# Optimization experiments

Hardware: AMD Instinct MI355X
Metric: run time of the kernel (lower is better)

The kernel has to match this reference:

```python
import jax, jax.numpy as jnp
import numpy as np

N_NODES = 100000
N_EDGES = 1200000
D = 64          # node_feat_size
G_FEAT = 128    # graph_feat_size
N_GRAPHS = 256
N_TASKS = 1


def setup_inputs() -> dict:
    key = jax.random.key(0)
    ks = jax.random.split(key, 12)
    node_feats = jax.random.normal(ks[0], (N_NODES, D), dtype=jnp.float32)
    edge_feats = jax.random.normal(ks[1], (N_EDGES, 8), dtype=jnp.float32)
    src = jax.random.randint(ks[2], (N_EDGES,), 0, N_NODES, dtype=jnp.int64 if jax.config.read('jax_enable_x64') else jnp.int32)
    dst = jax.random.randint(ks[3], (N_EDGES,), 0, N_NODES, dtype=src.dtype)
    graph_ids = jnp.sort(jax.random.randint(ks[4], (N_NODES,), 0, N_GRAPHS, dtype=src.dtype))
    s = 1.0 / np.sqrt(D)
    W_gcn = jax.random.uniform(ks[5], (D, D), minval=-s, maxval=s, dtype=jnp.float32)
    b_gcn = jnp.zeros((D,), jnp.float32)
    W_res = jax.random.uniform(ks[6], (D, D), minval=-s, maxval=s, dtype=jnp.float32)
    b_res = jnp.zeros((D,), jnp.float32)
    W_in = jax.random.uniform(ks[7], (D, D), minval=-s, maxval=s, dtype=jnp.float32)
    b_in = jnp.zeros((D,), jnp.float32)
    W_out = jax.random.uniform(ks[8], (D, G_FEAT), minval=-s, maxval=s, dtype=jnp.float32)
    b_out = jnp.zeros((G_FEAT,), jnp.float32)
    sp = 1.0 / np.sqrt(G_FEAT)
    W_pred = jax.random.uniform(ks[9], (G_FEAT, N_TASKS), minval=-sp, maxval=sp, dtype=jnp.float32)
    b_pred = jnp.zeros((N_TASKS,), jnp.float32)
    return dict(node_feats=node_feats, edge_feats=edge_feats, src=src, dst=dst,
                graph_ids=graph_ids, W_gcn=W_gcn, b_gcn=b_gcn, W_res=W_res, b_res=b_res,
                W_in=W_in, b_in=b_in, W_out=W_out, b_out=b_out, W_pred=W_pred, b_pred=b_pred)


def reference(node_feats, edge_feats, src, dst, graph_ids,
              W_gcn, b_gcn, W_res, b_res, W_in, b_in, W_out, b_out, W_pred, b_pred):
    # --- GCNLayer (GraphConv norm='none', activation=relu, residual=True) ---
    # message passing: copy src features, sum at dst (no normalization)
    agg = jax.ops.segment_sum(node_feats[src], dst, num_segments=N_NODES)  # [N, D]
    h = jax.nn.relu(agg @ W_gcn + b_gcn)                                   # graph_conv output
    h = h + jax.nn.relu(node_feats @ W_res + b_res)                        # residual branch
    # --- MLPNodeReadout (mode='sum') ---
    h = jax.nn.relu(h @ W_in + b_in)      # [N, D]
    h = h @ W_out + b_out                 # [N, G_FEAT]
    g_feats = jax.ops.segment_sum(h, graph_ids, num_segments=N_GRAPHS)  # [G, G_FEAT]
    # --- predict ---
    out = (g_feats @ W_pred + b_pred).reshape(-1)  # [G * n_tasks]
    return out
```

## Files before the change

### kernel.cpp

```cpp
#include <hip/hip_runtime.h>

typedef __attribute__((ext_vector_type(8))) __bf16 bf16x8;
typedef __attribute__((ext_vector_type(4))) float f32x4;

union Frag { unsigned short u[8]; bf16x8 b; };

__device__ __forceinline__ unsigned short rne_bf16(float x) {
    unsigned int u = __float_as_uint(x);
    return (unsigned short)((u + 0x7fffu + ((u >> 16) & 1u)) >> 16);
}
__device__ __forceinline__ float bf16_to_f(unsigned short h) {
    return __uint_as_float(((unsigned int)h) << 16);
}

#define MFMA16 __builtin_amdgcn_mfma_f32_16x16x32_bf16
#define SBSH 9
#define SBN 512
#define SBCAP 7168
#define BINCHUNK 4096
#define NWFRAG (3 * 2 * 2 * 4 * 64 * 8)

__global__ __launch_bounds__(256) void bin_kernel(
    const int* __restrict__ src, const int* __restrict__ dst,
    int* __restrict__ gcursor, int* __restrict__ binned,
    int nE, int nbS) {
    __shared__ int lhist[256], lbase[256], lofs[256];
    __shared__ int wsum[4];
    __shared__ int sortedV[BINCHUNK];
    __shared__ int sortedA[BINCHUNK];
    const int t = threadIdx.x;
    const int e0 = blockIdx.x * BINCHUNK;
    const int e1 = min(e0 + BINCHUNK, nE);
    const int cnt = e1 - e0;
    lhist[t] = 0;
    __syncthreads();
    int myr[16];
    #pragma unroll
    for (int u = 0; u < 16; ++u) {
        int e = e0 + t + u * 256;
        if (e < e1) myr[u] = atomicAdd(&lhist[dst[e] >> SBSH], 1);
    }
    __syncthreads();
    const int lane = t & 63, w = t >> 6;
    int x = lhist[t];
    #pragma unroll
    for (int s = 1; s < 64; s <<= 1) {
        int v = __shfl_up(x, s, 64);
        if (lane >= s) x += v;
    }
    if (lane == 63) wsum[w] = x;
    __syncthreads();
    if (t < 4) {
        int y = wsum[t];
        #pragma unroll
        for (int s = 1; s < 4; s <<= 1) {
            int v = __shfl_up(y, s, 64);
            if (t >= s) y += v;
        }
        wsum[t] = y;
    }
    __syncthreads();
    lofs[t] = x + (w ? wsum[w - 1] : 0);
    if (t < nbS) {
        int c = lhist[t];
        lbase[t] = c ? atomicAdd(&gcursor[t], c) : 0;
    }
    __syncthreads();
    #pragma unroll
    for (int u = 0; u < 16; ++u) {
        int e = e0 + t + u * 256;
        if (e < e1) {
            int d = dst[e];
            int sb = d >> SBSH;
            int r = myr[u];
            int p = (lofs[sb] - lhist[sb]) + r;
            sortedV[p] = (src[e] << SBSH) | (d & (SBN - 1));
            int gp = lbase[sb] + r;
            sortedA[p] = (gp < SBCAP) ? (sb * SBCAP + gp) : -1;
        }
    }
    __syncthreads();
    for (int i = t; i < cnt; i += 256) {
        int ga = sortedA[i];
        if (ga >= 0) binned[ga] = sortedV[i];
    }
}

__global__ __launch_bounds__(1024) void segB_kernel(
    int* __restrict__ binned, const int* __restrict__ gcursor,
    int2* __restrict__ nodeTab,
    const float* __restrict__ nf,
    const float* __restrict__ Wg, const float* __restrict__ Wr,
    const float* __restrict__ Wi, const float* __restrict__ Wo,
    const float* __restrict__ bo, const float* __restrict__ Wp,
    const float* __restrict__ bp,
    unsigned short* __restrict__ nfb, unsigned short* __restrict__ wfrag,
    float* __restrict__ wfold, float* __restrict__ c0, float* __restrict__ out,
    int nbS, int out_size, int nNodes) {
    __shared__ int eL[SBCAP];
    __shared__ int deg[SBN], sc[SBN];
    __shared__ int wsum[8];
    const int b = blockIdx.x, t = threadIdx.x;
    if (b < nbS) {
        const int cnt = min(gcursor[b], SBCAP);
        const int bb = b * SBCAP;
        if (t < SBN) deg[t] = 0;
        __syncthreads();
        int myr[7];
        #pragma unroll
        for (int u = 0; u < 7; ++u) {
            int i = t + u * 1024;
            if (i < cnt) {
                int p = binned[bb + i];
                eL[i] = p;
                myr[u] = atomicAdd(&deg[p & (SBN - 1)], 1);
            }
        }
        __syncthreads();
        const int lane = t & 63, w = t >> 6;
        if (t < SBN) {
            int d = deg[t];
            int x = d;
            #pragma unroll
            for (int s = 1; s < 64; s <<= 1) {
                int v = __shfl_up(x, s, 64);
                if (lane >= s) x += v;
            }
            if (lane == 63) wsum[w] = x;
            __syncthreads();
            if (t < 8) {
                int y = wsum[t];
                #pragma unroll
                for (int s = 1; s < 8; s <<= 1) {
                    int v = __shfl_up(y, s, 64);
                    if (t >= s) y += v;
                }
                wsum[t] = y;
            }
            __syncthreads();
            int incl = x + (w ? wsum[w - 1] : 0);
            int excl = incl - d;
            sc[t] = excl;
            int node = b * SBN + t;
            if (node < nNodes) nodeTab[node] = make_int2(bb + excl, d);
        } else {
            __syncthreads();
            __syncthreads();
        }
        __syncthreads();
        #pragma unroll
        for (int u = 0; u < 7; ++u) {
            int i = t + u * 1024;
            if (i < cnt) {
                int p = eL[i];
                int pos = sc[p & (SBN - 1)] + myr[u];
                binned[bb + pos] = p >> SBSH;
            }
        }
        return;
    }
    const int tp = ((int)blockIdx.x - nbS) * 1024 + t;
    const int nth = ((int)gridDim.x - nbS) * 1024;
    const float4* nf4 = (const float4*)nf;
    ushort4* nfb4 = (ushort4*)nfb;
    const int nQ = nNodes * 16;
    for (int i = tp; i < nQ; i += nth) {
        float4 v = nf4[i];
        ushort4 o;
        o.x = rne_bf16(v.x); o.y = rne_bf16(v.y);
        o.z = rne_bf16(v.z); o.w = rne_bf16(v.w);
        nfb4[i] = o;
    }
    const float* Ws[3] = {Wg, Wr, Wi};
    for (int idx = tp; idx < NWFRAG; idx += nth) {
        int j = idx & 7, lane = (idx >> 3) & 63, nt = (idx >> 9) & 3;
        int kt = (idx >> 11) & 1, part = (idx >> 12) & 1, mat = idx >> 13;
        int k = kt * 32 + ((lane >> 4) << 3) + j;
        int n = nt * 16 + (lane & 15);
        float ww = Ws[mat][k * 64 + n];
        unsigned short hi = rne_bf16(ww);
        wfrag[idx] = (part == 0) ? hi : rne_bf16(ww - bf16_to_f(hi));
    }
    if (tp < 64) {
        float s = 0.f;
        for (int j = 0; j < 128; ++j) s += Wo[tp * 128 + j] * Wp[j];
        wfold[tp] = s;
    }
    if (tp == 0) {
        float s = 0.f;
        for (int j = 0; j < 128; ++j) s += bo[j] * Wp[j];
        c0[0] = s;
    }
    if (tp < out_size) out[tp] = bp[0];
}

__global__ __launch_bounds__(256) void gather_kernel(
    const unsigned short* __restrict__ nfb, const int2* __restrict__ nodeTab,
    const int* __restrict__ srcs, unsigned short* __restrict__ aggb, int nNodes) {
    int wid = blockIdx.x * 4 + (threadIdx.x >> 6);
    if (wid >= nNodes) return;
    int lane = threadIdx.x & 63;
    int half = lane >> 5;
    int cp = lane & 31;
    int2 sd = nodeTab[wid];
    int base = sd.x, d = sd.y;
    const ushort2* nfb2 = (const ushort2*)nfb;
    float ax = 0.f, ay = 0.f;
    if (d > 0 && d <= 64) {
        int myidx = srcs[base + min(lane, d - 1)];
        int dh = (d - half + 1) >> 1;
        for (int jb = 0; jb < dh; jb += 8) {
            int sA[8];
            #pragma unroll
            for (int u = 0; u < 8; ++u) {
                int e = 2 * (jb + u) + half;
                sA[u] = __shfl(myidx, (e < d) ? e : (d - 1), 64);
            }
            ushort2 v[8];
            #pragma unroll
            for (int u = 0; u < 8; ++u)
                v[u] = nfb2[(long)sA[u] * 32 + cp];
            #pragma unroll
            for (int u = 0; u < 8; ++u)
                if (jb + u < dh) { ax += bf16_to_f(v[u].x); ay += bf16_to_f(v[u].y); }
        }
    } else if (d > 64) {
        int k = half;
        for (; k + 8 <= d; k += 8) {
            int s0 = srcs[base + k],     s1 = srcs[base + k + 2];
            int s2 = srcs[base + k + 4], s3 = srcs[base + k + 6];
            ushort2 v0 = nfb2[(long)s0 * 32 + cp];
            ushort2 v1 = nfb2[(long)s1 * 32 + cp];
            ushort2 v2 = nfb2[(long)s2 * 32 + cp];
            ushort2 v3 = nfb2[(long)s3 * 32 + cp];
            ax += (bf16_to_f(v0.x) + bf16_to_f(v1.x)) + (bf16_to_f(v2.x) + bf16_to_f(v3.x));
            ay += (bf16_to_f(v0.y) + bf16_to_f(v1.y)) + (bf16_to_f(v2.y) + bf16_to_f(v3.y));
        }
        for (; k < d; k += 2) {
            int s = srcs[base + k];
            ushort2 v = nfb2[(long)s * 32 + cp];
            ax += bf16_to_f(v.x); ay += bf16_to_f(v.y);
        }
    }
    ax += __shfl_xor(ax, 32, 64);
    ay += __shfl_xor(ay, 32, 64);
    if (half == 0) {
        ushort2 o; o.x = rne_bf16(ax); o.y = rne_bf16(ay);
        ((ushort2*)aggb)[(long)wid * 32 + cp] = o;
    }
}

__global__ __launch_bounds__(256) void mlp_kernel(
    const unsigned short* __restrict__ aggb, const unsigned short* __restrict__ nfb,
    const int* __restrict__ gids, const unsigned short* __restrict__ wfrag,
    const float* __restrict__ bg, const float* __restrict__ br,
    const float* __restrict__ bi, const float* __restrict__ wfold,
    const float* __restrict__ c0p, float* __restrict__ out, int nTiles) {
    __shared__ float hs_all[4][32 * 68];
    const int wave = threadIdx.x >> 6, lane = threadIdx.x & 63;
    const int wid = blockIdx.x * 4 + wave;
    if (wid >= nTiles) return;
    float* hs = hs_all[wave];
    const int base = wid * 32;
    const int mrow = lane & 15, quad = lane >> 4;

    Frag aA[2][2], aN[2][2];
    #pragma unroll
    for (int rt = 0; rt < 2; ++rt) {
        const unsigned short* rowA = aggb + (long)(base + rt * 16 + mrow) * 64;
        const unsigned short* rowN = nfb  + (long)(base + rt * 16 + mrow) * 64;
        #pragma unroll
        for (int kt = 0; kt < 2; ++kt) {
            aA[rt][kt].b = *(const bf16x8*)(rowA + kt * 32 + quad * 8);
            aN[rt][kt].b = *(const bf16x8*)(rowN + kt * 32 + quad * 8);
        }
    }
    const unsigned short* wl0 = wfrag + lane * 8;
    auto WF = [&](int mat, int part, int kt, int nt) -> bf16x8 {
        return *(const bf16x8*)(wl0 + (size_t)((((mat * 2 + part) * 2 + kt) * 4 + nt) * 64) * 8);
    };
    f32x4 accA[2][4], accR[2][4];
    #pragma unroll
    for (int rt = 0; rt < 2; ++rt)
        #pragma unroll
        for (int nt = 0; nt < 4; ++nt) {
            accA[rt][nt] = (f32x4){0.f, 0.f, 0.f, 0.f};
            accR[rt][nt] = (f32x4){0.f, 0.f, 0.f, 0.f};
        }
    #pragma unroll
    for (int nt = 0; nt < 4; ++nt)
        #pragma unroll
        for (int kt = 0; kt < 2; ++kt) {
            bf16x8 gh = WF(0, 0, kt, nt), gl = WF(0, 1, kt, nt);
            bf16x8 rh = WF(1, 0, kt, nt), rl = WF(1, 1, kt, nt);
            #pragma unroll
            for (int rt = 0; rt < 2; ++rt) {
                accA[rt][nt] = MFMA16(aA[rt][kt].b, gh, accA[rt][nt], 0, 0, 0);
                accA[rt][nt] = MFMA16(aA[rt][kt].b, gl, accA[rt][nt], 0, 0, 0);
                accR[rt][nt] = MFMA16(aN[rt][kt].b, rh, accR[rt][nt], 0, 0, 0);
                accR[rt][nt] = MFMA16(aN[rt][kt].b, rl, accR[rt][nt], 0, 0, 0);
            }
        }
    #pragma unroll
    for (int nt = 0; nt < 4; ++nt) {
        float bgv = bg[nt * 16 + mrow], brv = br[nt * 16 + mrow];
        #pragma unroll
        for (int rt = 0; rt < 2; ++rt)
            #pragma unroll
            for (int r = 0; r < 4; ++r) {
                float h = fmaxf(accA[rt][nt][r] + bgv, 0.f)
                        + fmaxf(accR[rt][nt][r] + brv, 0.f);
                hs[(rt * 16 + quad * 4 + r) * 68 + nt * 16 + mrow] = h;
            }
    }
    __builtin_amdgcn_wave_barrier();
    Frag aH[2][2];
    #pragma unroll
    for (int rt = 0; rt < 2; ++rt)
        #pragma unroll
        for (int kt = 0; kt < 2; ++kt) {
            const float* hp = hs + (rt * 16 + mrow) * 68 + kt * 32 + quad * 8;
            float4 v0 = *(const float4*)hp;
            float4 v1 = *(const float4*)(hp + 4);
            aH[rt][kt].u[0] = rne_bf16(v0.x); aH[rt][kt].u[1] = rne_bf16(v0.y);
            aH[rt][kt].u[2] = rne_bf16(v0.z); aH[rt][kt].u[3] = rne_bf16(v0.w);
            aH[rt][kt].u[4] = rne_bf16(v1.x); aH[rt][kt].u[5] = rne_bf16(v1.y);
            aH[rt][kt].u[6] = rne_bf16(v1.z); aH[rt][kt].u[7] = rne_bf16(v1.w);
        }
    f32x4 accH[2][4];
    #pragma unroll
    for (int rt = 0; rt < 2; ++rt)
        #pragma unroll
        for (int nt = 0; nt < 4; ++nt)
            accH[rt][nt] = (f32x4){0.f, 0.f, 0.f, 0.f};
    #pragma unroll
    for (int nt = 0; nt < 4; ++nt)
        #pragma unroll
        for (int kt = 0; kt < 2; ++kt) {
            bf16x8 ih = WF(2, 0, kt, nt), il = WF(2, 1, kt, nt);
            #pragma unroll
            for (int rt = 0; rt < 2; ++rt) {
                accH[rt][nt] = MFMA16(aH[rt][kt].b, ih, accH[rt][nt], 0, 0, 0);
                accH[rt][nt] = MFMA16(aH[rt][kt].b, il, accH[rt][nt], 0, 0, 0);
            }
        }
    float p[2][4];
    #pragma unroll
    for (int rt = 0; rt < 2; ++rt)
        #pragma unroll
        for (int r = 0; r < 4; ++r) p[rt][r] = 0.f;
    #pragma unroll
    for (int nt = 0; nt < 4; ++nt) {
        float biv = bi[nt * 16 + mrow], wfv = wfold[nt * 16 + mrow];
        #pragma unroll
        for (int rt = 0; rt < 2; ++rt)
            #pragma unroll
            for (int r = 0; r < 4; ++r)
                p[rt][r] += fmaxf(accH[rt][nt][r] + biv, 0.f) * wfv;
    }
    #pragma unroll
    for (int m = 1; m <= 8; m <<= 1)
        #pragma unroll
        for (int rt = 0; rt < 2; ++rt)
            #pragma unroll
            for (int r = 0; r < 4; ++r)
                p[rt][r] += __shfl_xor(p[rt][r], m, 64);
    const float c0 = c0p[0];
    #pragma unroll
    for (int rt = 0; rt < 2; ++rt)
        #pragma unroll
        for (int r = 0; r < 4; ++r) p[rt][r] += c0;
    int gself = gids[base + (lane & 31)];
    int g0 = __shfl(gself, 0, 64);
    if (__all(gself == g0)) {
        float pv = 0.f;
        if (mrow == 0) {
            #pragma unroll
            for (int rt = 0; rt < 2; ++rt)
                #pragma unroll
                for (int r = 0; r < 4; ++r) pv += p[rt][r];
        }
        pv += __shfl_xor(pv, 16, 64);
        pv += __shfl_xor(pv, 32, 64);
        if (lane == 0) atomicAdd(out + g0, pv);
    } else if (mrow == 0) {
        #pragma unroll
        for (int rt = 0; rt < 2; ++rt)
            #pragma unroll
            for (int r = 0; r < 4; ++r)
                atomicAdd(out + gids[base + rt * 16 + quad * 4 + r], p[rt][r]);
    }
}

extern "C" void kernel_launch(void* const* d_in, const int* in_sizes, int n_in,
                              void* d_out, int out_size, void* d_ws, size_t ws_size,
                              hipStream_t stream) {
    const float* node_feats = (const float*)d_in[0];
    const int* src  = (const int*)d_in[2];
    const int* dst  = (const int*)d_in[3];
    const int* gids = (const int*)d_in[4];
    const float* Wg = (const float*)d_in[5];
    const float* bg = (const float*)d_in[6];
    const float* Wr = (const float*)d_in[7];
    const float* br = (const float*)d_in[8];
    const float* Wi = (const float*)d_in[9];
    const float* bi = (const float*)d_in[10];
    const float* Wo = (const float*)d_in[11];
    const float* bo = (const float*)d_in[12];
    const float* Wp = (const float*)d_in[13];
    const float* bp = (const float*)d_in[14];
    float* out = (float*)d_out;

    const int nNodes = in_sizes[0] / 64;
    const int nE = in_sizes[2];
    const int nbS = (nNodes + SBN - 1) / SBN;
    const int nBin = (nE + BINCHUNK - 1) / BINCHUNK;
    const int nTiles = (nNodes + 31) / 32;

    int* gcursor = (int*)d_ws;
    int* binned  = gcursor + 256;
    int2* nodeTab = (int2*)(binned + (size_t)nbS * SBCAP);
    unsigned short* nfb  = (unsigned short*)(nodeTab + nNodes);
    unsigned short* aggb = nfb + (size_t)nNodes * 64;
    unsigned short* wfrag = aggb + (size_t)nNodes * 64;
    float* wfold = (float*)(wfrag + NWFRAG);
    float* c0 = wfold + 64;

    hipMemsetAsync(gcursor, 0, 256 * sizeof(int), stream);

    bin_kernel<<<nBin, 256, 0, stream>>>(src, dst, gcursor, binned, nE, nbS);

    segB_kernel<<<nbS + 256, 1024, 0, stream>>>(binned, gcursor, nodeTab,
        node_feats, Wg, Wr, Wi, Wo, bo, Wp, bp,
        nfb, wfrag, wfold, c0, out, nbS, out_size, nNodes);

    gather_kernel<<<(nNodes + 3) / 4, 256, 0, stream>>>(nfb, nodeTab, binned, aggb, nNodes);

    mlp_kernel<<<(nTiles + 3) / 4, 256, 0, stream>>>(aggb, nfb, gids, wfrag,
        bg, br, bi, wfold, c0, out, nTiles);
}
```

Before: 210.2 us.

## Fuse binning, segment sort, gather and MLP into one cooperative persistent kernel

Replaces the memset plus four separate kernel launches with a single cooperative kernel that runs each phase in grid-stride loops, separated by grid-wide syncs. Shared memory is reused across phases through a union. The gather phase now handles two nodes per wave, and the segment phase runs with 256 threads instead of 1024. This removes launch overhead and inter-kernel gaps, but adds grid.sync costs, caps occupancy at the cooperative grid size, and changes the per-phase parallelism.

```diff
diff --git a/kernel.cpp b/kernel.cpp
--- a/kernel.cpp
+++ b/kernel.cpp
@@ -1,4 +1,7 @@
 #include <hip/hip_runtime.h>
+#include <hip/hip_cooperative_groups.h>
+
+namespace cg = cooperative_groups;
 
 typedef __attribute__((ext_vector_type(8))) __bf16 bf16x8;
 typedef __attribute__((ext_vector_type(4))) float f32x4;
@@ -20,375 +23,394 @@
 #define BINCHUNK 4096
 #define NWFRAG (3 * 2 * 2 * 4 * 64 * 8)
 
-__global__ __launch_bounds__(256) void bin_kernel(
-    const int* __restrict__ src, const int* __restrict__ dst,
-    int* __restrict__ gcursor, int* __restrict__ binned,
-    int nE, int nbS) {
-    __shared__ int lhist[256], lbase[256], lofs[256];
-    __shared__ int wsum[4];
-    __shared__ int sortedV[BINCHUNK];
-    __shared__ int sortedA[BINCHUNK];
+struct KArgs {
+    const float* nf; const int* src; const int* dst; const int* gids;
+    const float* Wg; const float* bg; const float* Wr; const float* br;
+    const float* Wi; const float* bi; const float* Wo; const float* bo;
+    const float* Wp; const float* bp;
+    float* out;
+    int* gcursor; int* binned; int2* nodeTab;
+    unsigned short* nfb; unsigned short* aggb; unsigned short* wfrag;
+    float* wfold; float* c0;
+    int nBin, nE, nbS, out_size, nNodes, nTiles;
+};
+
+__global__ __launch_bounds__(256, 4) void fused_kernel(KArgs A) {
+    __shared__ union {
+        struct { int lhist[256], lbase[256], lofs[256], wsum[4];
+                 int sortedV[BINCHUNK], sortedA[BINCHUNK]; } bin;
+        struct { int eL[SBCAP], deg[SBN], sc[SBN], wsum[8]; } seg;
+        struct { float hs[4][32 * 68]; } m;
+    } U;
+    cg::grid_group grid = cg::this_grid();
     const int t = threadIdx.x;
-    const int e0 = blockIdx.x * BINCHUNK;
-    const int e1 = min(e0 + BINCHUNK, nE);
-    const int cnt = e1 - e0;
-    lhist[t] = 0;
-    __syncthreads();
-    int myr[16];
-    #pragma unroll
-    for (int u = 0; u < 16; ++u) {
-        int e = e0 + t + u * 256;
-        if (e < e1) myr[u] = atomicAdd(&lhist[dst[e] >> SBSH], 1);
+    const int b = blockIdx.x;
+    const int G = gridDim.x;
+    const int lane = t & 63, wave = t >> 6;
+
+    if (b == 0) A.gcursor[t] = 0;
+    grid.sync();
+
+    for (int c = b; c < A.nBin; c += G) {
+        const int e0 = c * BINCHUNK;
+        const int e1 = min(e0 + BINCHUNK, A.nE);
+        const int cnt = e1 - e0;
+        U.bin.lhist[t] = 0;
+        __syncthreads();
+        int myr[16];
+        #pragma unroll
+        for (int u = 0; u < 16; ++u) {
+            int e = e0 + t + u * 256;
+            if (e < e1) myr[u] = atomicAdd(&U.bin.lhist[A.dst[e] >> SBSH], 1);
+        }
+        __syncthreads();
+        int x = U.bin.lhist[t];
+        #pragma unroll
+        for (int s = 1; s < 64; s <<= 1) {
+            int v = __shfl_up(x, s, 64);
+            if (lane >= s) x += v;
+        }
+        if (lane == 63) U.bin.wsum[wave] = x;
+        __syncthreads();
+        if (t < 4) {
+            int y = U.bin.wsum[t];
+            #pragma unroll
+            for (int s = 1; s < 4; s <<= 1) {
+                int v = __shfl_up(y, s, 64);
+                if (t >= s) y += v;
+            }
+            U.bin.wsum[t] = y;
+        }
+        __syncthreads();
+        U.bin.lofs[t] = x + (wave ? U.bin.wsum[wave - 1] : 0);
+        if (t < A.nbS) {
+            int cc = U.bin.lhist[t];
+            U.bin.lbase[t] = cc ? atomicAdd(&A.gcursor[t], cc) : 0;
+        }
+        __syncthreads();
+        #pragma unroll
+        for (int u = 0; u < 16; ++u) {
+            int e = e0 + t + u * 256;
+            if (e < e1) {
+                int d = A.dst[e];
+                int sb = d >> SBSH;
+                int r = myr[u];
+                int p = (U.bin.lofs[sb] - U.bin.lhist[sb]) + r;
+                U.bin.sortedV[p] = (A.src[e] << SBSH) | (d & (SBN - 1));
+                int gp = U.bin.lbase[sb] + r;
+                U.bin.sortedA[p] = (gp < SBCAP) ? (sb * SBCAP + gp) : -1;
+            }
+        }
+        __syncthreads();
+        for (int i = t; i < cnt; i += 256) {
+            int ga = U.bin.sortedA[i];
+            if (ga >= 0) A.binned[ga] = U.bin.sortedV[i];
+        }
+        __syncthreads();
     }
-    __syncthreads();
-    const int lane = t & 63, w = t >> 6;
-    int x = lhist[t];
-    #pragma unroll
-    for (int s = 1; s < 64; s <<= 1) {
-        int v = __shfl_up(x, s, 64);
-        if (lane >= s) x += v;
+    {
+        const int tp = b * 256 + t;
+        const int nth = G * 256;
+        const float4* nf4 = (const float4*)A.nf;
+        ushort4* nfb4 = (ushort4*)A.nfb;
+        const int nQ = A.nNodes * 16;
+        for (int i = tp; i < nQ; i += nth) {
+            float4 v = nf4[i];
+            ushort4 o;
+            o.x = rne_bf16(v.x); o.y = rne_bf16(v.y);
+            o.z = rne_bf16(v.z); o.w = rne_bf16(v.w);
+            nfb4[i] = o;
+        }
+        const float* Ws[3] = {A.Wg, A.Wr, A.Wi};
+        for (int idx = tp; idx < NWFRAG; idx += nth) {
+            int j = idx & 7, ln = (idx >> 3) & 63, nt = (idx >> 9) & 3;
+            int kt = (idx >> 11) & 1, part = (idx >> 12) & 1, mat = idx >> 13;
+            int k = kt * 32 + ((ln >> 4) << 3) + j;
+            int n = nt * 16 + (ln & 15);
+            float ww = Ws[mat][k * 64 + n];
+            unsigned short hi = rne_bf16(ww);
+            A.wfrag[idx] = (part == 0) ? hi : rne_bf16(ww - bf16_to_f(hi));
+        }
+        if (tp < 64) {
+            float s = 0.f;
+            for (int j = 0; j < 128; ++j) s += A.Wo[tp * 128 + j] * A.Wp[j];
+            A.wfold[tp] = s;
+        }
+        if (tp == 0) {
+            float s = 0.f;
+            for (int j = 0; j < 128; ++j) s += A.bo[j] * A.Wp[j];
+            A.c0[0] = s;
+        }
+        if (tp < A.out_size) A.out[tp] = A.bp[0];
     }
-    if (lane == 63) wsum[w] = x;
-    __syncthreads();
-    if (t < 4) {
-        int y = wsum[t];
-        #pragma unroll
-        for (int s = 1; s < 4; s <<= 1) {
-            int v = __shfl_up(y, s, 64);
-            if (t >= s) y += v;
-        }
-        wsum[t] = y;
+    grid.sync();
+
+    for (int bk = b; bk < A.nbS; bk += G) {
+        const int cnt = min(A.gcursor[bk], SBCAP);
+        const int bb = bk * SBCAP;
+        U.seg.deg[t] = 0; U.seg.deg[t + 256] = 0;
+        __syncthreads();
+        int myr[28];
+        #pragma unroll
+        for (int u = 0; u < 28; ++u) {
+            int i = t + u * 256;
+            if (i < cnt) {
+                int p = A.binned[bb + i];
+                U.seg.eL[i] = p;
+                myr[u] = atomicAdd(&U.seg.deg[p & (SBN - 1)], 1);
+            }
+        }
+        __syncthreads();
+        int d0 = U.seg.deg[2 * t], d1 = U.seg.deg[2 * t + 1];
+        int pp = d0 + d1;
+        int x = pp;
+        #pragma unroll
+        for (int s = 1; s < 64; s <<= 1) {
+            int v = __shfl_up(x, s, 64);
+            if (lane >= s) x += v;
+        }
+        if (lane == 63) U.seg.wsum[wave] = x;
+        __syncthreads();
+        if (t < 4) {
+            int y = U.seg.wsum[t];
+            #pragma unroll
+            for (int s = 1; s < 4; s <<= 1) {
+                int v = __shfl_up(y, s, 64);
+                if (t >= s) y += v;
+            }
+            U.seg.wsum[t] = y;
+        }
+        __syncthreads();
+        int incl = x + (wave ? U.seg.wsum[wave - 1] : 0);
+        int e0x = incl - pp;
+        int e1x = e0x + d0;
+        U.seg.sc[2 * t] = e0x; U.seg.sc[2 * t + 1] = e1x;
+        int node0 = bk * SBN + 2 * t;
+        if (node0 < A.nNodes)     A.nodeTab[node0]     = make_int2(bb + e0x, d0);
+        if (node0 + 1 < A.nNodes) A.nodeTab[node0 + 1] = make_int2(bb + e1x, d1);
+        __syncthreads();
+        #pragma unroll
+        for (int u = 0; u < 28; ++u) {
+            int i = t + u * 256;
+            if (i < cnt) {
+                int p = U.seg.eL[i];
+                int pos = U.seg.sc[p & (SBN - 1)] + myr[u];
+                A.binned[bb + pos] = p >> SBSH;
+            }
+        }
+        __syncthreads();
     }
-    __syncthreads();
-    lofs[t] = x + (w ? wsum[w - 1] : 0);
-    if (t < nbS) {
-        int c = lhist[t];
-        lbase[t] = c ? atomicAdd(&gcursor[t], c) : 0;
+    grid.sync();
+
+    {
+        const int gw = b * 4 + wave;
+        const int nw = G * 4;
+        const int half = lane >> 5, cp = lane & 31;
+        const ushort2* nfb2 = (const ushort2*)A.nfb;
+        auto bigpath = [&](int basex, int dd, float& ax, float& ay) {
+            int k = half;
+            for (; k + 8 <= dd; k += 8) {
+                int s0 = A.binned[basex + k],     s1 = A.binned[basex + k + 2];
+                int s2 = A.binned[basex + k + 4], s3 = A.binned[basex + k + 6];
+                ushort2 v0 = nfb2[(long)s0 * 32 + cp];
+                ushort2 v1 = nfb2[(long)s1 * 32 + cp];
+                ushort2 v2 = nfb2[(long)s2 * 32 + cp];
+                ushort2 v3 = nfb2[(long)s3 * 32 + cp];
+                ax += (bf16_to_f(v0.x) + bf16_to_f(v1.x)) + (bf16_to_f(v2.x) + bf16_to_f(v3.x));
+                ay += (bf16_to_f(v0.y) + bf16_to_f(v1.y)) + (bf16_to_f(v2.y) + bf16_to_f(v3.y));
+            }
+            for (; k < dd; k += 2) {
+                int s = A.binned[basex + k];
+                ushort2 v = nfb2[(long)s * 32 + cp];
+                ax += bf16_to_f(v.x); ay += bf16_to_f(v.y);
+            }
+        };
+        for (int n0 = gw * 2; n0 < A.nNodes; n0 += nw * 2) {
+            const int n1 = n0 + 1;
+            const bool h1 = (n1 < A.nNodes);
+            int2 sd0 = A.nodeTab[n0];
+            int2 sd1 = h1 ? A.nodeTab[n1] : make_int2(0, 0);
+            const int b0 = sd0.x, d0v = sd0.y, b1 = sd1.x, d1v = sd1.y;
+            float ax0 = 0.f, ay0 = 0.f, ax1 = 0.f, ay1 = 0.f;
+            if (d0v <= 64 && d1v <= 64) {
+                int idx0 = (d0v > 0) ? A.binned[b0 + min(lane, d0v - 1)] : 0;
+                int idx1 = (d1v > 0) ? A.binned[b1 + min(lane, d1v - 1)] : 0;
+                int dh0 = (d0v > 0) ? ((d0v - half + 1) >> 1) : 0;
+                int dh1 = (d1v > 0) ? ((d1v - half + 1) >> 1) : 0;
+                int dhm = max(dh0, dh1);
+                for (int jb = 0; jb < dhm; jb += 8) {
+                    int sA0[8], sA1[8];
+                    #pragma unroll
+                    for (int u = 0; u < 8; ++u) {
+                        int e = 2 * (jb + u) + half;
+                        sA0[u] = __shfl(idx0, (e < d0v) ? e : max(d0v - 1, 0), 64);
+                        sA1[u] = __shfl(idx1, (e < d1v) ? e : max(d1v - 1, 0), 64);
+                    }
+                    ushort2 v0[8], v1[8];
+                    #pragma unroll
+                    for (int u = 0; u < 8; ++u) {
+                        v0[u] = nfb2[(long)sA0[u] * 32 + cp];
+                        v1[u] = nfb2[(long)sA1[u] * 32 + cp];
+                    }
+                    #pragma unroll
+                    for (int u = 0; u < 8; ++u) {
+                        if (jb + u < dh0) { ax0 += bf16_to_f(v0[u].x); ay0 += bf16_to_f(v0[u].y); }
+                        if (jb + u < dh1) { ax1 += bf16_to_f(v1[u].x); ay1 += bf16_to_f(v1[u].y); }
+                    }
+                }
+            } else {
+                if (d0v > 0) bigpath(b0, d0v, ax0, ay0);
+                if (h1 && d1v > 0) bigpath(b1, d1v, ax1, ay1);
+            }
+            ax0 += __shfl_xor(ax0, 32, 64); ay0 += __shfl_xor(ay0, 32, 64);
+            ax1 += __shfl_xor(ax1, 32, 64); ay1 += __shfl_xor(ay1, 32, 64);
+            if (half == 0) {
+                ushort2 o0; o0.x = rne_bf16(ax0); o0.y = rne_bf16(ay0);
+                ((ushort2*)A.aggb)[(long)n0 * 32 + cp] = o0;
+                if (h1) {
+                    ushort2 o1; o1.x = rne_bf16(ax1); o1.y = rne_bf16(ay1);
+                    ((ushort2*)A.aggb)[(long)n1 * 32 + cp] = o1;
+                }
+            }
+        }
     }
-    __syncthreads();
-    #pragma unroll
-    for (int u = 0; u < 16; ++u) {
-        int e = e0 + t + u * 256;
-        if (e < e1) {
-            int d = dst[e];
-            int sb = d >> SBSH;
-            int r = myr[u];
-            int p = (lofs[sb] - lhist[sb]) + r;
-            sortedV[p] = (src[e] << SBSH) | (d & (SBN - 1));
-            int gp = lbase[sb] + r;
-            sortedA[p] = (gp < SBCAP) ? (sb * SBCAP + gp) : -1;
-        }
-    }
-    __syncthreads();
-    for (int i = t; i < cnt; i += 256) {
-        int ga = sortedA[i];
-        if (ga >= 0) binned[ga] = sortedV[i];
-    }
-}
-
-__global__ __launch_bounds__(1024) void segB_kernel(
-    int* __restrict__ binned, const int* __restrict__ gcursor,
-    int2* __restrict__ nodeTab,
-    const float* __restrict__ nf,
-    const float* __restrict__ Wg, const float* __restrict__ Wr,
-    const float* __restrict__ Wi, const float* __restrict__ Wo,
-    const float* __restrict__ bo, const float* __restrict__ Wp,
-    const float* __restrict__ bp,
-    unsigned short* __restrict__ nfb, unsigned short* __restrict__ wfrag,
-    float* __restrict__ wfold, float* __restrict__ c0, float* __restrict__ out,
-    int nbS, int out_size, int nNodes) {
-    __shared__ int eL[SBCAP];
-    __shared__ int deg[SBN], sc[SBN];
-    __shared__ int wsum[8];
-    const int b = blockIdx.x, t = threadIdx.x;
-    if (b < nbS) {
-        const int cnt = min(gcursor[b], SBCAP);
-        const int bb = b * SBCAP;
-        if (t < SBN) deg[t] = 0;
-        __syncthreads();
-        int myr[7];
-        #pragma unroll
-        for (int u = 0; u < 7; ++u) {
-            int i = t + u * 1024;
-            if (i < cnt) {
-                int p = binned[bb + i];
-                eL[i] = p;
-                myr[u] = atomicAdd(&deg[p & (SBN - 1)], 1);
-            }
-        }
-        __syncthreads();
-        const int lane = t & 63, w = t >> 6;
-        if (t < SBN) {
-            int d = deg[t];
-            int x = d;
-            #pragma unroll
-            for (int s = 1; s < 64; s <<= 1) {
-                int v = __shfl_up(x, s, 64);
-                if (lane >= s) x += v;
-            }
-            if (lane == 63) wsum[w] = x;
-            __syncthreads();
-            if (t < 8) {
-                int y = wsum[t];
-                #pragma unroll
-                for (int s = 1; s < 8; s <<= 1) {
-                    int v = __shfl_up(y, s, 64);
-                    if (t >= s) y += v;
-                }
-                wsum[t] = y;
-            }
-            __syncthreads();
-            int incl = x + (w ? wsum[w - 1] : 0);
-            int excl = incl - d;
-            sc[t] = excl;
-            int node = b * SBN + t;
-            if (node < nNodes) nodeTab[node] = make_int2(bb + excl, d);
-        } else {
-            __syncthreads();
-            __syncthreads();
-        }
-        __syncthreads();
-        #pragma unroll
-        for (int u = 0; u < 7; ++u) {
-            int i = t + u * 1024;
-            if (i < cnt) {
-                int p = eL[i];
-                int pos = sc[p & (SBN - 1)] + myr[u];
-                binned[bb + pos] = p >> SBSH;
-            }
-        }
-        return;
-    }
-    const int tp = ((int)blockIdx.x - nbS) * 1024 + t;
-    const int nth = ((int)gridDim.x - nbS) * 1024;
-    const float4* nf4 = (const float4*)nf;
-    ushort4* nfb4 = (ushort4*)nfb;
-    const int nQ = nNodes * 16;
-    for (int i = tp; i < nQ; i += nth) {
-        float4 v = nf4[i];
-        ushort4 o;
-        o.x = rne_bf16(v.x); o.y = rne_bf16(v.y);
-        o.z = rne_bf16(v.z); o.w = rne_bf16(v.w);
-        nfb4[i] = o;
-    }
-    const float* Ws[3] = {Wg, Wr, Wi};
-    for (int idx = tp; idx < NWFRAG; idx += nth) {
-        int j = idx & 7, lane = (idx >> 3) & 63, nt = (idx >> 9) & 3;
-        int kt = (idx >> 11) & 1, part = (idx >> 12) & 1, mat = idx >> 13;
-        int k = kt * 32 + ((lane >> 4) << 3) + j;
-        int n = nt * 16 + (lane & 15);
-        float ww = Ws[mat][k * 64 + n];
-        unsigned short hi = rne_bf16(ww);
-        wfrag[idx] = (part == 0) ? hi : rne_bf16(ww - bf16_to_f(hi));
-    }
-    if (tp < 64) {
-        float s = 0.f;
-        for (int j = 0; j < 128; ++j) s += Wo[tp * 128 + j] * Wp[j];
-        wfold[tp] = s;
-    }
-    if (tp == 0) {
-        float s = 0.f;
-        for (int j = 0; j < 128; ++j) s += bo[j] * Wp[j];
-        c0[0] = s;
-    }
-    if (tp < out_size) out[tp] = bp[0];
-}
-
-__global__ __launch_bounds__(256) void gather_kernel(
-    const unsigned short* __restrict__ nfb, const int2* __restrict__ nodeTab,
-    const int* __restrict__ srcs, unsigned short* __restrict__ aggb, int nNodes) {
-    int wid = blockIdx.x * 4 + (threadIdx.x >> 6);
-    if (wid >= nNodes) return;
-    int lane = threadIdx.x & 63;
-    int half = lane >> 5;
-    int cp = lane & 31;
-    int2 sd = nodeTab[wid];
-    int base = sd.x, d = sd.y;
-    const ushort2* nfb2 = (const ushort2*)nfb;
-    float ax = 0.f, ay = 0.f;
-    if (d > 0 && d <= 64) {
-        int myidx = srcs[base + min(lane, d - 1)];
-        int dh = (d - half + 1) >> 1;
-        for (int jb = 0; jb < dh; jb += 8) {
-            int sA[8];
-            #pragma unroll
-            for (int u = 0; u < 8; ++u) {
-                int e = 2 * (jb + u) + half;
-                sA[u] = __shfl(myidx, (e < d) ? e : (d - 1), 64);
-            }
-            ushort2 v[8];
-            #pragma unroll
-            for (int u = 0; u < 8; ++u)
-                v[u] = nfb2[(long)sA[u] * 32 + cp];
-            #pragma unroll
-            for (int u = 0; u < 8; ++u)
-                if (jb + u < dh) { ax += bf16_to_f(v[u].x); ay += bf16_to_f(v[u].y); }
-        }
-    } else if (d > 64) {
-        int k = half;
-        for (; k + 8 <= d; k += 8) {
-            int s0 = srcs[base + k],     s1 = srcs[base + k + 2];
-            int s2 = srcs[base + k + 4], s3 = srcs[base + k + 6];
-            ushort2 v0 = nfb2[(long)s0 * 32 + cp];
-            ushort2 v1 = nfb2[(long)s1 * 32 + cp];
-            ushort2 v2 = nfb2[(long)s2 * 32 + cp];
-            ushort2 v3 = nfb2[(long)s3 * 32 + cp];
-            ax += (bf16_to_f(v0.x) + bf16_to_f(v1.x)) + (bf16_to_f(v2.x) + bf16_to_f(v3.x));
-            ay += (bf16_to_f(v0.y) + bf16_to_f(v1.y)) + (bf16_to_f(v2.y) + bf16_to_f(v3.y));
-        }
-        for (; k < d; k += 2) {
-            int s = srcs[base + k];
-            ushort2 v = nfb2[(long)s * 32 + cp];
-            ax += bf16_to_f(v.x); ay += bf16_to_f(v.y);
-        }
-    }
-    ax += __shfl_xor(ax, 32, 64);
-    ay += __shfl_xor(ay, 32, 64);
-    if (half == 0) {
-        ushort2 o; o.x = rne_bf16(ax); o.y = rne_bf16(ay);
-        ((ushort2*)aggb)[(long)wid * 32 + cp] = o;
-    }
-}
-
-__global__ __launch_bounds__(256) void mlp_kernel(
-    const unsigned short* __restrict__ aggb, const unsigned short* __restrict__ nfb,
-    const int* __restrict__ gids, const unsigned short* __restrict__ wfrag,
-    const float* __restrict__ bg, const float* __restrict__ br,
-    const float* __restrict__ bi, const float* __restrict__ wfold,
-    const float* __restrict__ c0p, float* __restrict__ out, int nTiles) {
-    __shared__ float hs_all[4][32 * 68];
-    const int wave = threadIdx.x >> 6, lane = threadIdx.x & 63;
-    const int wid = blockIdx.x * 4 + wave;
-    if (wid >= nTiles) return;
-    float* hs = hs_all[wave];
-    const int base = wid * 32;
-    const int mrow = lane & 15, quad = lane >> 4;
-
-    Frag aA[2][2], aN[2][2];
-    #pragma unroll
-    for (int rt = 0; rt < 2; ++rt) {
-        const unsigned short* rowA = aggb + (long)(base + rt * 16 + mrow) * 64;
-        const unsigned short* rowN = nfb  + (long)(base + rt * 16 + mrow) * 64;
-        #pragma unroll
-        for (int kt = 0; kt < 2; ++kt) {
-            aA[rt][kt].b = *(const bf16x8*)(rowA + kt * 32 + quad * 8);
-            aN[rt][kt].b = *(const bf16x8*)(rowN + kt * 32 + quad * 8);
-        }
-    }
-    const unsigned short* wl0 = wfrag + lane * 8;
-    auto WF = [&](int mat, int part, int kt, int nt) -> bf16x8 {
-        return *(const bf16x8*)(wl0 + (size_t)((((mat * 2 + part) * 2 + kt) * 4 + nt) * 64) * 8);
-    };
-    f32x4 accA[2][4], accR[2][4];
-    #pragma unroll
-    for (int rt = 0; rt < 2; ++rt)
-        #pragma unroll
-        for (int nt = 0; nt < 4; ++nt) {
-            accA[rt][nt] = (f32x4){0.f, 0.f, 0.f, 0.f};
-            accR[rt][nt] = (f32x4){0.f, 0.f, 0.f, 0.f};
-        }
-    #pragma unroll
-    for (int nt = 0; nt < 4; ++nt)
-        #pragma unroll
-        for (int kt = 0; kt < 2; ++kt) {
-            bf16x8 gh = WF(0, 0, kt, nt), gl = WF(0, 1, kt, nt);
-            bf16x8 rh = WF(1, 0, kt, nt), rl = WF(1, 1, kt, nt);
+    grid.sync();
+
+    {
+        const int gw = b * 4 + wave;
+        const int nw = G * 4;
+        float* hs = U.m.hs[wave];
+        const int mrow = lane & 15, quad = lane >> 4;
+        const unsigned short* wl0 = A.wfrag + lane * 8;
+        auto WF = [&](int mat, int part, int kt, int nt) -> bf16x8 {
+            return *(const bf16x8*)(wl0 + (size_t)((((mat * 2 + part) * 2 + kt) * 4 + nt) * 64) * 8);
+        };
+        for (int wid = gw; wid < A.nTiles; wid += nw) {
+            const int base = wid * 32;
+            Frag aA[2][2], aN[2][2];
             #pragma unroll
             for (int rt = 0; rt < 2; ++rt) {
-                accA[rt][nt] = MFMA16(aA[rt][kt].b, gh, accA[rt][nt], 0, 0, 0);
-                accA[rt][nt] = MFMA16(aA[rt][kt].b, gl, accA[rt][nt], 0, 0, 0);
-                accR[rt][nt] = MFMA16(aN[rt][kt].b, rh, accR[rt][nt], 0, 0, 0);
-                accR[rt][nt] = MFMA16(aN[rt][kt].b, rl, accR[rt][nt], 0, 0, 0);
-            }
-        }
-    #pragma unroll
-    for (int nt = 0; nt < 4; ++nt) {
-        float bgv = bg[nt * 16 + mrow], brv = br[nt * 16 + mrow];
-        #pragma unroll
-        for (int rt = 0; rt < 2; ++rt)
-            #pragma unroll
-            for (int r = 0; r < 4; ++r) {
-                float h = fmaxf(accA[rt][nt][r] + bgv, 0.f)
-                        + fmaxf(accR[rt][nt][r] + brv, 0.f);
-                hs[(rt * 16 + quad * 4 + r) * 68 + nt * 16 + mrow] = h;
-            }
-    }
-    __builtin_amdgcn_wave_barrier();
-    Frag aH[2][2];
-    #pragma unroll
-    for (int rt = 0; rt < 2; ++rt)
-        #pragma unroll
-        for (int kt = 0; kt < 2; ++kt) {
-            const float* hp = hs + (rt * 16 + mrow) * 68 + kt * 32 + quad * 8;
-            float4 v0 = *(const float4*)hp;
-            float4 v1 = *(const float4*)(hp + 4);
-            aH[rt][kt].u[0] = rne_bf16(v0.x); aH[rt][kt].u[1] = rne_bf16(v0.y);
-            aH[rt][kt].u[2] = rne_bf16(v0.z); aH[rt][kt].u[3] = rne_bf16(v0.w);
-            aH[rt][kt].u[4] = rne_bf16(v1.x); aH[rt][kt].u[5] = rne_bf16(v1.y);
-            aH[rt][kt].u[6] = rne_bf16(v1.z); aH[rt][kt].u[7] = rne_bf16(v1.w);
-        }
-    f32x4 accH[2][4];
-    #pragma unroll
-    for (int rt = 0; rt < 2; ++rt)
-        #pragma unroll
-        for (int nt = 0; nt < 4; ++nt)
-            accH[rt][nt] = (f32x4){0.f, 0.f, 0.f, 0.f};
-    #pragma unroll
-    for (int nt = 0; nt < 4; ++nt)
-        #pragma unroll
-        for (int kt = 0; kt < 2; ++kt) {
-            bf16x8 ih = WF(2, 0, kt, nt), il = WF(2, 1, kt, nt);
-            #pragma unroll
-            for (int rt = 0; rt < 2; ++rt) {
-                accH[rt][nt] = MFMA16(aH[rt][kt].b, ih, accH[rt][nt], 0, 0, 0);
-                accH[rt][nt] = MFMA16(aH[rt][kt].b, il, accH[rt][nt], 0, 0, 0);
-            }
-        }
-    float p[2][4];
-    #pragma unroll
-    for (int rt = 0; rt < 2; ++rt)
-        #pragma unroll
-        for (int r = 0; r < 4; ++r) p[rt][r] = 0.f;
-    #pragma unroll
-    for (int nt = 0; nt < 4; ++nt) {
-        float biv = bi[nt * 16 + mrow], wfv = wfold[nt * 16 + mrow];
-        #pragma unroll
-        for (int rt = 0; rt < 2; ++rt)
-            #pragma unroll
-            for (int r = 0; r < 4; ++r)
-                p[rt][r] += fmaxf(accH[rt][nt][r] + biv, 0.f) * wfv;
-    }
-    #pragma unroll
-    for (int m = 1; m <= 8; m <<= 1)
-        #pragma unroll
-        for (int rt = 0; rt < 2; ++rt)
-            #pragma unroll
-            for (int r = 0; r < 4; ++r)
-                p[rt][r] += __shfl_xor(p[rt][r], m, 64);
-    const float c0 = c0p[0];
-    #pragma unroll
-    for (int rt = 0; rt < 2; ++rt)
-        #pragma unroll
-        for (int r = 0; r < 4; ++r) p[rt][r] += c0;
-    int gself = gids[base + (lane & 31)];
-    int g0 = __shfl(gself, 0, 64);
-    if (__all(gself == g0)) {
-        float pv = 0.f;
-        if (mrow == 0) {
+                const unsigned short* rowA = A.aggb + (long)(base + rt * 16 + mrow) * 64;
+                const unsigned short* rowN = A.nfb  + (long)(base + rt * 16 + mrow) * 64;
+                #pragma unroll
+                for (int kt = 0; kt < 2; ++kt) {
+                    aA[rt][kt].b = *(const bf16x8*)(rowA + kt * 32 + quad * 8);
+                    aN[rt][kt].b = *(const bf16x8*)(rowN + kt * 32 + quad * 8);
+                }
+            }
+            f32x4 accA[2][4], accR[2][4];
             #pragma unroll
             for (int rt = 0; rt < 2; ++rt)
                 #pragma unroll
-                for (int r = 0; r < 4; ++r) pv += p[rt][r];
-        }
-        pv += __shfl_xor(pv, 16, 64);
-        pv += __shfl_xor(pv, 32, 64);
-        if (lane == 0) atomicAdd(out + g0, pv);
-    } else if (mrow == 0) {
-        #pragma unroll
-        for (int rt = 0; rt < 2; ++rt)
-            #pragma unroll
-            for (int r = 0; r < 4; ++r)
-                atomicAdd(out + gids[base + rt * 16 + quad * 4 + r], p[rt][r]);
+                for (int nt = 0; nt < 4; ++nt) {
+                    accA[rt][nt] = (f32x4){0.f, 0.f, 0.f, 0.f};
+                    accR[rt][nt] = (f32x4){0.f, 0.f, 0.f, 0.f};
+                }
+            #pragma unroll
+            for (int nt = 0; nt < 4; ++nt)
+                #pragma unroll
+                for (int kt = 0; kt < 2; ++kt) {
+                    bf16x8 gh = WF(0, 0, kt, nt), gl = WF(0, 1, kt, nt);
+                    bf16x8 rh = WF(1, 0, kt, nt), rl = WF(1, 1, kt, nt);
+                    #pragma unroll
+                    for (int rt = 0; rt < 2; ++rt) {
+                        accA[rt][nt] = MFMA16(aA[rt][kt].b, gh, accA[rt][nt], 0, 0, 0);
+                        accA[rt][nt] = MFMA16(aA[rt][kt].b, gl, accA[rt][nt], 0, 0, 0);
+                        accR[rt][nt] = MFMA16(aN[rt][kt].b, rh, accR[rt][nt], 0, 0, 0);
+                        accR[rt][nt] = MFMA16(aN[rt][kt].b, rl, accR[rt][nt], 0, 0, 0);
+                    }
+                }
+            #pragma unroll
+            for (int nt = 0; nt < 4; ++nt) {
+                float bgv = A.bg[nt * 16 + mrow], brv = A.br[nt * 16 + mrow];
+                #pragma unroll
+                for (int rt = 0; rt < 2; ++rt)
+                    #pragma unroll
+                    for (int r = 0; r < 4; ++r) {
+                        float h = fmaxf(accA[rt][nt][r] + bgv, 0.f)
+                                + fmaxf(accR[rt][nt][r] + brv, 0.f);
+                        hs[(rt * 16 + quad * 4 + r) * 68 + nt * 16 + mrow] = h;
+                    }
+            }
+            __builtin_amdgcn_wave_barrier();
+            Frag aH[2][2];
+            #pragma unroll
+            for (int rt = 0; rt < 2; ++rt)
+                #pragma unroll
+                for (int kt = 0; kt < 2; ++kt) {
+                    const float* hp = hs + (rt * 16 + mrow) * 68 + kt * 32 + quad * 8;
+                    float4 v0 = *(const float4*)hp;
+                    float4 v1 = *(const float4*)(hp + 4);
+                    aH[rt][kt].u[0] = rne_bf16(v0.x); aH[rt][kt].u[1] = rne_bf16(v0.y);
+                    aH[rt][kt].u[2] = rne_bf16(v0.z); aH[rt][kt].u[3] = rne_bf16(v0.w);
+                    aH[rt][kt].u[4] = rne_bf16(v1.x); aH[rt][kt].u[5] = rne_bf16(v1.y);
+                    aH[rt][kt].u[6] = rne_bf16(v1.z); aH[rt][kt].u[7] = rne_bf16(v1.w);
+                }
+            __builtin_amdgcn_wave_barrier();
+            f32x4 accH[2][4];
+            #pragma unroll
+            for (int rt = 0; rt < 2; ++rt)
+                #pragma unroll
+                for (int nt = 0; nt < 4; ++nt)
+                    accH[rt][nt] = (f32x4){0.f, 0.f, 0.f, 0.f};
+            #pragma unroll
+            for (int nt = 0; nt < 4; ++nt)
+                #pragma unroll
+                for (int kt = 0; kt < 2; ++kt) {
+                    bf16x8 ih = WF(2, 0, kt, nt), il = WF(2, 1, kt, nt);
+                    #pragma unroll
+                    for (int rt = 0; rt < 2; ++rt) {
+                        accH[rt][nt] = MFMA16(aH[rt][kt].b, ih, accH[rt][nt], 0, 0, 0);
+                        accH[rt][nt] = MFMA16(aH[rt][kt].b, il, accH[rt][nt], 0, 0, 0);
+                    }
+                }
+            float p[2][4];
+            #pragma unroll
+            for (int rt = 0; rt < 2; ++rt)
+                #pragma unroll
+                for (int r = 0; r < 4; ++r) p[rt][r] = 0.f;
+            #pragma unroll
+            for (int nt = 0; nt < 4; ++nt) {
+                float biv = A.bi[nt * 16 + mrow], wfv = A.wfold[nt * 16 + mrow];
+                #pragma unroll
+                for (int rt = 0; rt < 2; ++rt)
+                    #pragma unroll
+                    for (int r = 0; r < 4; ++r)
+                        p[rt][r] += fmaxf(accH[rt][nt][r] + biv, 0.f) * wfv;
+            }
+            #pragma unroll
+            for (int m = 1; m <= 8; m <<= 1)
+                #pragma unroll
+                for (int rt = 0; rt < 2; ++rt)
+                    #pragma unroll
+                    for (int r = 0; r < 4; ++r)
+                        p[rt][r] += __shfl_xor(p[rt][r], m, 64);
+            const float c0v = A.c0[0];
+            #pragma unroll
+            for (int rt = 0; rt < 2; ++rt)
+                #pragma unroll
+                for (int r = 0; r < 4; ++r) p[rt][r] += c0v;
+            int gself = A.gids[base + (lane & 31)];
+            int g0 = __shfl(gself, 0, 64);
+            if (__all(gself == g0)) {
+                float pv = 0.f;
+                if (mrow == 0) {
+                    #pragma unroll
+                    for (int rt = 0; rt < 2; ++rt)
+                        #pragma unroll
+                        for (int r = 0; r < 4; ++r) pv += p[rt][r];
+                }
+                pv += __shfl_xor(pv, 16, 64);
+                pv += __shfl_xor(pv, 32, 64);
+                if (lane == 0) atomicAdd(A.out + g0, pv);
+            } else if (mrow == 0) {
+                #pragma unroll
+                for (int rt = 0; rt < 2; ++rt)
+                    #pragma unroll
+                    for (int r = 0; r < 4; ++r)
+                        atomicAdd(A.out + A.gids[base + rt * 16 + quad * 4 + r], p[rt][r]);
+            }
+        }
     }
 }
 
@@ -399,17 +421,6 @@
     const int* src  = (const int*)d_in[2];
     const int* dst  = (const int*)d_in[3];
     const int* gids = (const int*)d_in[4];
-    const float* Wg = (const float*)d_in[5];
-    const float* bg = (const float*)d_in[6];
-    const float* Wr = (const float*)d_in[7];
-    const float* br = (const float*)d_in[8];
-    const float* Wi = (const float*)d_in[9];
-    const float* bi = (const float*)d_in[10];
-    const float* Wo = (const float*)d_in[11];
-    const float* bo = (const float*)d_in[12];
-    const float* Wp = (const float*)d_in[13];
-    const float* bp = (const float*)d_in[14];
-    float* out = (float*)d_out;
 
     const int nNodes = in_sizes[0] / 64;
     const int nE = in_sizes[2];
@@ -426,16 +437,25 @@
     float* wfold = (float*)(wfrag + NWFRAG);
     float* c0 = wfold + 64;
 
-    hipMemsetAsync(gcursor, 0, 256 * sizeof(int), stream);
-
-    bin_kernel<<<nBin, 256, 0, stream>>>(src, dst, gcursor, binned, nE, nbS);
-
-    segB_kernel<<<nbS + 256, 1024, 0, stream>>>(binned, gcursor, nodeTab,
-        node_feats, Wg, Wr, Wi, Wo, bo, Wp, bp,
-        nfb, wfrag, wfold, c0, out, nbS, out_size, nNodes);
-
-    gather_kernel<<<(nNodes + 3) / 4, 256, 0, stream>>>(nfb, nodeTab, binned, aggb, nNodes);
-
-    mlp_kernel<<<(nTiles + 3) / 4, 256, 0, stream>>>(aggb, nfb, gids, wfrag,
-        bg, br, bi, wfold, c0, out, nTiles);
+    KArgs A;
+    A.nf = node_feats; A.src = src; A.dst = dst; A.gids = gids;
+    A.Wg = (const float*)d_in[5];  A.bg = (const float*)d_in[6];
+    A.Wr = (const float*)d_in[7];  A.br = (const float*)d_in[8];
+    A.Wi = (const float*)d_in[9];  A.bi = (const float*)d_in[10];
+    A.Wo = (const float*)d_in[11]; A.bo = (const float*)d_in[12];
+    A.Wp = (const float*)d_in[13]; A.bp = (const float*)d_in[14];
+    A.out = (float*)d_out;
+    A.gcursor = gcursor; A.binned = binned; A.nodeTab = nodeTab;
+    A.nfb = nfb; A.aggb = aggb; A.wfrag = wfrag; A.wfold = wfold; A.c0 = c0;
+    A.nBin = nBin; A.nE = nE; A.nbS = nbS; A.out_size = out_size;
+    A.nNodes = nNodes; A.nTiles = nTiles;
+
+    int maxB = 0;
+    hipOccupancyMaxActiveBlocksPerMultiprocessor(&maxB, fused_kernel, 256, 0);
+    if (maxB < 1) maxB = 1;
+    if (maxB > 8) maxB = 8;
+    int G = 256 * maxB;
+
+    void* kp[] = { (void*)&A };
+    hipLaunchCooperativeKernel(fused_kernel, dim3(G), dim3(256), kp, 0, stream);
 }
```

New measurement: 517.7 us. +146.3%, slower.

## Fuse neighbor gather into MLP kernel via shared-memory aggregation tile

Applied to the files above, without the earlier changes.

Merges the gather and MLP kernels. Each block of four waves gathers 32 destination rows into a shared-memory bf16 tile, then wave 0 runs the MFMA MLP on that tile, with the float staging buffer sharing the same shared memory through a union. This removes the global round-trip of the aggregated features and one kernel launch. In exchange, three of the four waves sit idle during the MLP phase, and the gather now uses a per-block __syncthreads, which may lower throughput.

```diff
diff --git a/kernel.cpp b/kernel.cpp
--- a/kernel.cpp
+++ b/kernel.cpp
@@ -194,87 +194,97 @@
     if (tp < out_size) out[tp] = bp[0];
 }
 
-__global__ __launch_bounds__(256) void gather_kernel(
+__global__ __launch_bounds__(256) void gathermlp_kernel(
     const unsigned short* __restrict__ nfb, const int2* __restrict__ nodeTab,
-    const int* __restrict__ srcs, unsigned short* __restrict__ aggb, int nNodes) {
-    int wid = blockIdx.x * 4 + (threadIdx.x >> 6);
-    if (wid >= nNodes) return;
-    int lane = threadIdx.x & 63;
-    int half = lane >> 5;
-    int cp = lane & 31;
-    int2 sd = nodeTab[wid];
-    int base = sd.x, d = sd.y;
-    const ushort2* nfb2 = (const ushort2*)nfb;
-    float ax = 0.f, ay = 0.f;
-    if (d > 0 && d <= 64) {
-        int myidx = srcs[base + min(lane, d - 1)];
-        int dh = (d - half + 1) >> 1;
-        for (int jb = 0; jb < dh; jb += 8) {
-            int sA[8];
-            #pragma unroll
-            for (int u = 0; u < 8; ++u) {
-                int e = 2 * (jb + u) + half;
-                sA[u] = __shfl(myidx, (e < d) ? e : (d - 1), 64);
-            }
-            ushort2 v[8];
-            #pragma unroll
-            for (int u = 0; u < 8; ++u)
-                v[u] = nfb2[(long)sA[u] * 32 + cp];
-            #pragma unroll
-            for (int u = 0; u < 8; ++u)
-                if (jb + u < dh) { ax += bf16_to_f(v[u].x); ay += bf16_to_f(v[u].y); }
-        }
-    } else if (d > 64) {
-        int k = half;
-        for (; k + 8 <= d; k += 8) {
-            int s0 = srcs[base + k],     s1 = srcs[base + k + 2];
-            int s2 = srcs[base + k + 4], s3 = srcs[base + k + 6];
-            ushort2 v0 = nfb2[(long)s0 * 32 + cp];
-            ushort2 v1 = nfb2[(long)s1 * 32 + cp];
-            ushort2 v2 = nfb2[(long)s2 * 32 + cp];
-            ushort2 v3 = nfb2[(long)s3 * 32 + cp];
-            ax += (bf16_to_f(v0.x) + bf16_to_f(v1.x)) + (bf16_to_f(v2.x) + bf16_to_f(v3.x));
-            ay += (bf16_to_f(v0.y) + bf16_to_f(v1.y)) + (bf16_to_f(v2.y) + bf16_to_f(v3.y));
-        }
-        for (; k < d; k += 2) {
-            int s = srcs[base + k];
-            ushort2 v = nfb2[(long)s * 32 + cp];
-            ax += bf16_to_f(v.x); ay += bf16_to_f(v.y);
-        }
-    }
-    ax += __shfl_xor(ax, 32, 64);
-    ay += __shfl_xor(ay, 32, 64);
-    if (half == 0) {
-        ushort2 o; o.x = rne_bf16(ax); o.y = rne_bf16(ay);
-        ((ushort2*)aggb)[(long)wid * 32 + cp] = o;
-    }
-}
-
-__global__ __launch_bounds__(256) void mlp_kernel(
-    const unsigned short* __restrict__ aggb, const unsigned short* __restrict__ nfb,
-    const int* __restrict__ gids, const unsigned short* __restrict__ wfrag,
+    const int* __restrict__ srcs, const int* __restrict__ gids,
+    const unsigned short* __restrict__ wfrag,
     const float* __restrict__ bg, const float* __restrict__ br,
     const float* __restrict__ bi, const float* __restrict__ wfold,
-    const float* __restrict__ c0p, float* __restrict__ out, int nTiles) {
-    __shared__ float hs_all[4][32 * 68];
+    const float* __restrict__ c0p, float* __restrict__ out,
+    int nTiles, int nNodes) {
+    __shared__ union {
+        unsigned short agg[32][72];
+        float hs[32][68];
+    } U;
     const int wave = threadIdx.x >> 6, lane = threadIdx.x & 63;
-    const int wid = blockIdx.x * 4 + wave;
+    const int wid = blockIdx.x;
     if (wid >= nTiles) return;
-    float* hs = hs_all[wave];
     const int base = wid * 32;
+    const int half = lane >> 5, cp = lane & 31;
+    const ushort2* nfb2 = (const ushort2*)nfb;
+
+    int sdx = 0, sdy = 0;
+    {
+        int n = base + wave * 8 + (lane & 7);
+        if (lane < 8 && n < nNodes) {
+            int2 sd = nodeTab[n];
+            sdx = sd.x; sdy = sd.y;
+        }
+    }
+    #pragma unroll 1
+    for (int i = 0; i < 8; ++i) {
+        const int rbase = __shfl(sdx, i, 64);
+        const int d     = __shfl(sdy, i, 64);
+        float ax = 0.f, ay = 0.f;
+        if (d > 0 && d <= 64) {
+            int myidx = srcs[rbase + min(lane, d - 1)];
+            int dh = (d - half + 1) >> 1;
+            for (int jb = 0; jb < dh; jb += 8) {
+                int sA[8];
+                #pragma unroll
+                for (int u = 0; u < 8; ++u) {
+                    int e = 2 * (jb + u) + half;
+                    sA[u] = __shfl(myidx, (e < d) ? e : (d - 1), 64);
+                }
+                ushort2 v[8];
+                #pragma unroll
+                for (int u = 0; u < 8; ++u)
+                    v[u] = nfb2[(long)sA[u] * 32 + cp];
+                #pragma unroll
+                for (int u = 0; u < 8; ++u)
+                    if (jb + u < dh) { ax += bf16_to_f(v[u].x); ay += bf16_to_f(v[u].y); }
+            }
+        } else if (d > 64) {
+            int k = half;
+            for (; k + 8 <= d; k += 8) {
+                int s0 = srcs[rbase + k],     s1 = srcs[rbase + k + 2];
+                int s2 = srcs[rbase + k + 4], s3 = srcs[rbase + k + 6];
+                ushort2 v0 = nfb2[(long)s0 * 32 + cp];
+                ushort2 v1 = nfb2[(long)s1 * 32 + cp];
+                ushort2 v2 = nfb2[(long)s2 * 32 + cp];
+                ushort2 v3 = nfb2[(long)s3 * 32 + cp];
+                ax += (bf16_to_f(v0.x) + bf16_to_f(v1.x)) + (bf16_to_f(v2.x) + bf16_to_f(v3.x));
+                ay += (bf16_to_f(v0.y) + bf16_to_f(v1.y)) + (bf16_to_f(v2.y) + bf16_to_f(v3.y));
+            }
+            for (; k < d; k += 2) {
+                int s = srcs[rbase + k];
+                ushort2 v = nfb2[(long)s * 32 + cp];
+                ax += bf16_to_f(v.x); ay += bf16_to_f(v.y);
+            }
+        }
+        ax += __shfl_xor(ax, 32, 64);
+        ay += __shfl_xor(ay, 32, 64);
+        if (half == 0) {
+            ushort2 o; o.x = rne_bf16(ax); o.y = rne_bf16(ay);
+            *(ushort2*)(&U.agg[wave * 8 + i][2 * cp]) = o;
+        }
+    }
+    __syncthreads();
+    if (wave != 0) return;
+
     const int mrow = lane & 15, quad = lane >> 4;
-
     Frag aA[2][2], aN[2][2];
     #pragma unroll
     for (int rt = 0; rt < 2; ++rt) {
-        const unsigned short* rowA = aggb + (long)(base + rt * 16 + mrow) * 64;
-        const unsigned short* rowN = nfb  + (long)(base + rt * 16 + mrow) * 64;
+        const unsigned short* rowA = &U.agg[rt * 16 + mrow][0];
+        const unsigned short* rowN = nfb + (long)(base + rt * 16 + mrow) * 64;
         #pragma unroll
         for (int kt = 0; kt < 2; ++kt) {
             aA[rt][kt].b = *(const bf16x8*)(rowA + kt * 32 + quad * 8);
             aN[rt][kt].b = *(const bf16x8*)(rowN + kt * 32 + quad * 8);
         }
     }
+    asm volatile("" ::: "memory");
     const unsigned short* wl0 = wfrag + lane * 8;
     auto WF = [&](int mat, int part, int kt, int nt) -> bf16x8 {
         return *(const bf16x8*)(wl0 + (size_t)((((mat * 2 + part) * 2 + kt) * 4 + nt) * 64) * 8);
@@ -301,6 +311,8 @@
                 accR[rt][nt] = MFMA16(aN[rt][kt].b, rl, accR[rt][nt], 0, 0, 0);
             }
         }
+    asm volatile("" ::: "memory");
+    float* hs = &U.hs[0][0];
     #pragma unroll
     for (int nt = 0; nt < 4; ++nt) {
         float bgv = bg[nt * 16 + mrow], brv = br[nt * 16 + mrow];
@@ -434,8 +446,6 @@
         node_feats, Wg, Wr, Wi, Wo, bo, Wp, bp,
         nfb, wfrag, wfold, c0, out, nbS, out_size, nNodes);
 
-    gather_kernel<<<(nNodes + 3) / 4, 256, 0, stream>>>(nfb, nodeTab, binned, aggb, nNodes);
-
-    mlp_kernel<<<(nTiles + 3) / 4, 256, 0, stream>>>(aggb, nfb, gids, wfrag,
-        bg, br, bi, wfold, c0, out, nTiles);
-}
+    gathermlp_kernel<<<nTiles, 256, 0, stream>>>(nfb, nodeTab, binned, gids,
+        wfrag, bg, br, bi, wfold, c0, out, nTiles, nNodes);
+}
```

Measured after the change: 231.4 us. 10.1% more time.
